# Kernel optimization log

Measured on AMD Instinct MI355X. Metric: run time of the kernel, lower is better.

## Reference

```python
import jax, jax.numpy as jnp
import numpy as np

NUM_EXECUTORS = 50
NUM_DAG_FEATURES = 3
EMB_DAG = 16
EMB_GLOB = 16
HIDDEN = [64, 64, 32]
B = 60000            # number of jobs (one per env in the batched rollout)
NODES_PER_JOB = 10
NODE_FEAT = 5


def _init_mlp(key, dims):
    ws, bs = [], []
    for i in range(len(dims) - 1):
        key, k = jax.random.split(key)
        scale = 1.0 / np.sqrt(dims[i])
        ws.append(jax.random.uniform(k, (dims[i], dims[i + 1]), jnp.float32, -scale, scale))
        bs.append(jnp.zeros((dims[i + 1],), jnp.float32))
    return ws, bs


def setup_inputs() -> dict:
    rng = np.random.default_rng(0)
    n_nodes = B * NODES_PER_JOB
    # dag_batch.ptr: job i owns nodes [i*NODES_PER_JOB, (i+1)*NODES_PER_JOB)
    ptr = np.arange(B + 1, dtype=np.int64) * NODES_PER_JOB
    job_indices = rng.permutation(B).astype(np.int64)
    # ragged action counts per job (exec_mask is a prefix mask of length num_exec_acts[i])
    num_exec_acts = rng.integers(1, NUM_EXECUTORS + 1, size=B).astype(np.int64)
    n_sel = num_exec_acts[job_indices]
    T = int(n_sel.sum())
    # per-ragged-row executor index: concat([arange(n) for n in n_sel]), vectorized
    starts = np.cumsum(n_sel) - n_sel
    exec_act_idx = (np.arange(T, dtype=np.int64) - np.repeat(starts, n_sel)).astype(np.int64)

    key = jax.random.key(0)
    k_x, k_hd, k_hg, k_mlp = jax.random.split(key, 4)
    x = jax.random.normal(k_x, (n_nodes, NODE_FEAT), jnp.float32)
    h_dag = jax.random.normal(k_hd, (B, EMB_DAG), jnp.float32)
    h_glob = jax.random.normal(k_hg, (B, EMB_GLOB), jnp.float32)

    in_dim = NUM_DAG_FEATURES + EMB_DAG + EMB_GLOB + 1  # 36
    ws, bs = _init_mlp(k_mlp, [in_dim] + HIDDEN + [1])

    return {
        "x": x,
        "h_dag": h_dag,
        "h_glob": h_glob,
        "ptr": jnp.asarray(ptr),
        "job_indices": jnp.asarray(job_indices),
        "num_exec_acts": jnp.asarray(num_exec_acts),
        "exec_act_idx": jnp.asarray(exec_act_idx),
        "W1": ws[0], "b1": bs[0],
        "W2": ws[1], "b2": bs[1],
        "W3": ws[2], "b3": bs[2],
        "W4": ws[3], "b4": bs[3],
    }


def reference(x, h_dag, h_glob, ptr, job_indices, num_exec_acts, exec_act_idx,
              W1, b1, W2, b2, W3, b3, W4, b4):
    T = exec_act_idx.shape[0]                       # total ragged action rows (static)
    J = job_indices.shape[0]
    # masked gather: dag features at each dag's start node, then select jobs
    x_dag = x[ptr[:-1], :NUM_DAG_FEATURES][job_indices]        # [J, 3]
    h_dag_sel = h_dag[job_indices]                              # [J, 16]
    x_h_dag = jnp.concatenate([x_dag, h_dag_sel], axis=1)       # [J, 19]
    # variable repeat_interleave -> gather by repeated row index
    n_sel = num_exec_acts[job_indices]
    rpt = jnp.repeat(jnp.arange(J), n_sel, total_repeat_length=T)
    x_h_rpt = x_h_dag[rpt]                                      # [T, 19]
    h_glob_rpt = h_glob[rpt]                                    # [T, 16]
    # exec action feature: k / num_executors for the k-th valid executor
    exec_actions = (exec_act_idx.astype(x.dtype) / NUM_EXECUTORS)[:, None]  # [T, 1]
    h = jnp.concatenate([x_h_rpt, h_glob_rpt, exec_actions], axis=1)        # [T, 36]
    h = jax.nn.relu(h @ W1 + b1)
    h = jax.nn.relu(h @ W2 + b2)
    h = jax.nn.relu(h @ W3 + b3)
    scores = (h @ W4 + b4).squeeze(-1)                          # [T]
    return scores
```

## Files before the change

### kernel.cpp

```cpp
#include <hip/hip_runtime.h>

#define TPB 256

using half8  = __attribute__((ext_vector_type(8))) _Float16;
using fp16x2 = __attribute__((ext_vector_type(2))) __fp16;
using hv2    = __attribute__((ext_vector_type(2))) _Float16;
using f32x4  = __attribute__((ext_vector_type(4))) float;

static __device__ __forceinline__ unsigned pkrtz(float a, float b) {
    fp16x2 h = __builtin_amdgcn_cvt_pkrtz(a, b);
    return __builtin_bit_cast(unsigned, h);
}
static __device__ __forceinline__ hv2 pk2(float a, float b) {
    fp16x2 h = __builtin_amdgcn_cvt_pkrtz(a, b);
    return __builtin_bit_cast(hv2, h);
}
template <int CTRL>
static __device__ __forceinline__ float dppmov(float x) {
    return __int_as_float(__builtin_amdgcn_mov_dpp(__float_as_int(x), CTRL, 0xF, 0xF, true));
}
#define DPP_SWAP 0xB1

__global__ __launch_bounds__(TPB) void k_prep(const float* __restrict__ x,
                                              const float* __restrict__ h_dag,
                                              const float* __restrict__ h_glob,
                                              const int* __restrict__ ptr,
                                              const int* __restrict__ job_indices,
                                              const int* __restrict__ num_exec_acts,
                                              int J, int nb,
                                              unsigned* __restrict__ s16,
                                              int* __restrict__ bsum, int* __restrict__ jsv,
                                              const float* __restrict__ W1,
                                              const float* __restrict__ b1,
                                              const float* __restrict__ W2,
                                              const float* __restrict__ b2,
                                              const float* __restrict__ W3,
                                              const float* __restrict__ b3,
                                              const float* __restrict__ W4,
                                              uint4* __restrict__ wfrag,
                                              float4* __restrict__ bfrag)
{
    if (blockIdx.x == (unsigned)(4 * nb)) {
        if (threadIdx.x < 64) {
            int lane = threadIdx.x;
            int n = lane & 15, q = lane >> 4;
#pragma unroll
            for (int nt = 0; nt < 4; nt++) {
#pragma unroll
                for (int s = 0; s < 2; s++) {
                    half8 w2f;
#pragma unroll
                    for (int jj = 0; jj < 8; jj++) {
                        int ks = s * 32 + q * 8 + jj;
                        w2f[jj] = (_Float16)W2[ks * 64 + nt * 16 + n];
                    }
                    wfrag[(8 + nt * 2 + s) * 64 + lane] = __builtin_bit_cast(uint4, w2f);
                }
            }
#pragma unroll
            for (int nt = 0; nt < 2; nt++) {
#pragma unroll
                for (int s = 0; s < 2; s++) {
                    half8 w3f;
#pragma unroll
                    for (int jj = 0; jj < 8; jj++) {
                        int ks = s * 32 + q * 8 + jj;
                        w3f[jj] = (_Float16)W3[ks * 32 + nt * 16 + n];
                    }
                    wfrag[(16 + nt * 2 + s) * 64 + lane] = __builtin_bit_cast(uint4, w3f);
                }
            }
            bfrag[1 * 64 + lane] = make_float4(b2[n], b2[16 + n], b2[32 + n], b2[48 + n]);
            bfrag[2 * 64 + lane] = make_float4(b3[n], b3[16 + n], W4[n], W4[16 + n]);
        }
        return;
    }

    const int qtr = blockIdx.x / nb;
    const int cb  = blockIdx.x - qtr * nb;
    int j = cb * TPB + threadIdx.x;
    int v = 0;
    if (j < J) {
        int ji   = job_indices[j];
        if (qtr == 0) v = num_exec_acts[ji];
        int node = ptr[ji];
        float f[35];
        f[0] = x[node * 5 + 0];
        f[1] = x[node * 5 + 1];
        f[2] = x[node * 5 + 2];
        float4 hd[4], hg[4];
#pragma unroll
        for (int c4 = 0; c4 < 4; c4++) hd[c4] = *(const float4*)(h_dag + (size_t)ji * 16 + 4 * c4);
#pragma unroll
        for (int c4 = 0; c4 < 4; c4++) hg[c4] = *(const float4*)(h_glob + (size_t)j * 16 + 4 * c4);
#pragma unroll
        for (int c4 = 0; c4 < 4; c4++) {
            f[3 + 4 * c4 + 0]  = hd[c4].x; f[3 + 4 * c4 + 1]  = hd[c4].y;
            f[3 + 4 * c4 + 2]  = hd[c4].z; f[3 + 4 * c4 + 3]  = hd[c4].w;
            f[19 + 4 * c4 + 0] = hg[c4].x; f[19 + 4 * c4 + 1] = hg[c4].y;
            f[19 + 4 * c4 + 2] = hg[c4].z; f[19 + 4 * c4 + 3] = hg[c4].w;
        }
        float acc[16];
#pragma unroll
        for (int d4 = 0; d4 < 4; d4++) {
            float4 b = *(const float4*)(b1 + qtr * 16 + 4 * d4);
            acc[4 * d4 + 0] = b.x; acc[4 * d4 + 1] = b.y;
            acc[4 * d4 + 2] = b.z; acc[4 * d4 + 3] = b.w;
        }
#pragma unroll
        for (int c = 0; c < 35; c++) {
            float fc = f[c];
#pragma unroll
            for (int d4 = 0; d4 < 4; d4++) {
                float4 w = *(const float4*)(W1 + c * 64 + qtr * 16 + 4 * d4);
                acc[4 * d4 + 0] += fc * w.x; acc[4 * d4 + 1] += fc * w.y;
                acc[4 * d4 + 2] += fc * w.z; acc[4 * d4 + 3] += fc * w.w;
            }
        }
        unsigned* dst = s16 + ((size_t)qtr * J + j) * 8;
        ((uint4*)dst)[0] = make_uint4(pkrtz(acc[0], acc[1]),  pkrtz(acc[2], acc[3]),
                                      pkrtz(acc[4], acc[5]),  pkrtz(acc[6], acc[7]));
        ((uint4*)dst)[1] = make_uint4(pkrtz(acc[8], acc[9]),  pkrtz(acc[10], acc[11]),
                                      pkrtz(acc[12], acc[13]), pkrtz(acc[14], acc[15]));
    }
    if (qtr != 0) return;

    __shared__ int sc[TPB];
    sc[threadIdx.x] = v;
    __syncthreads();
    for (int d = 1; d < TPB; d <<= 1) {
        int add = (threadIdx.x >= d) ? sc[threadIdx.x - d] : 0;
        __syncthreads();
        sc[threadIdx.x] += add;
        __syncthreads();
    }
    if (j < J) jsv[j] = ((sc[threadIdx.x] - v) << 6) | v;
    if (threadIdx.x == TPB - 1) bsum[cb] = sc[TPB - 1];
}

__global__ __launch_bounds__(TPB) void k_mlp_mfma(const unsigned* __restrict__ s16,
                                                  const float* __restrict__ W1,
                                                  const int* __restrict__ jsv,
                                                  const int* __restrict__ bsum,
                                                  const uint4* __restrict__ wfrag,
                                                  const float4* __restrict__ bfrag,
                                                  const float* __restrict__ b4,
                                                  float* __restrict__ out,
                                                  int T, int J, int nb, int numTiles, int chunk)
{
    __shared__ __align__(16) char smem[4 * 4096];
    __shared__ int boffs[TPB];
    __shared__ int swin[4][64];
    __shared__ int srow[4][64];
    const int tid  = threadIdx.x;
    const int lane = tid & 63;
    const int wv   = tid >> 6;
    const int n    = lane & 15;
    const int q    = lane >> 4;
    char* slab = smem + wv * 4096;

    {
        int v = (tid < nb) ? bsum[tid] : 0;
        boffs[tid] = v;
        __syncthreads();
        for (int d = 1; d < TPB; d <<= 1) {
            int add = (tid >= d) ? boffs[tid - d] : 0;
            __syncthreads();
            boffs[tid] += add;
            __syncthreads();
        }
        int ex = boffs[tid] - v;
        __syncthreads();
        boffs[tid] = ex;
        __syncthreads();
    }

    half8 bw2[4][2], bw3[2][2];
#pragma unroll
    for (int nt = 0; nt < 4; nt++)
#pragma unroll
        for (int s = 0; s < 2; s++)
            bw2[nt][s] = __builtin_bit_cast(half8, wfrag[(8 + nt * 2 + s) * 64 + lane]);
#pragma unroll
    for (int nt = 0; nt < 2; nt++)
#pragma unroll
        for (int s = 0; s < 2; s++)
            bw3[nt][s] = __builtin_bit_cast(half8, wfrag[(16 + nt * 2 + s) * 64 + lane]);

    float4 bf2 = bfrag[1 * 64 + lane];
    float4 bf3 = bfrag[2 * 64 + lane];
    float bb2[4] = {bf2.x, bf2.y, bf2.z, bf2.w};
    float bb3[2] = {bf3.x, bf3.y};
    const float w4a = bf3.z, w4b = bf3.w;
    const float b4v = b4[0];
    const int   swr = (n >> 1) & 7;
    const int   odd = n & 1;

    hv2 w36p[8];
    {
        const float* wp = W1 + 35 * 64 + q * 8;
#pragma unroll
        for (int k = 0; k < 4; k++) w36p[k]     = pk2(wp[2 * k],      wp[2 * k + 1]);
#pragma unroll
        for (int k = 0; k < 4; k++) w36p[4 + k] = pk2(wp[32 + 2 * k], wp[32 + 2 * k + 1]);
    }
    const hv2 z2 = {(_Float16)0.0f, (_Float16)0.0f};

    const uint4* sbLo = (const uint4*)s16 + ((size_t)(q >> 1) * J) * 2 + (q & 1);
    const uint4* sbHi = (const uint4*)s16 + ((size_t)(2 + (q >> 1)) * J) * 2 + (q & 1);

    const int t0 = blockIdx.x * chunk;
    const int t1 = (t0 + chunk < numTiles) ? (t0 + chunk) : numTiles;
    const int R  = (t1 - t0) * 32;
    const int r0 = t0 * 128 + wv * R;
    int rend = r0 + R;
    if (rend > T) rend = T;

    if (r0 < rend) {
        int j_lo;
        {
            int lo = 0, hi = nb - 1;
            while (lo < hi) {
                int mid = (lo + hi + 1) >> 1;
                if (boffs[mid] <= r0) lo = mid; else hi = mid - 1;
            }
            j_lo = lo << 8;
        }
        int sreg    = 0;
        int win_top = 0x80000000;

        half8 a2[2][2];

        auto build_a2 = [&](int mtbase) {
#pragma unroll
            for (int m = 0; m < 2; m++) {
                int u   = srow[wv][16 * (mtbase + m) + n];
                int job = u >> 8;
                float e = (float)(u & 255) * 0.02f;
                uint4 lo = sbLo[(size_t)job * 2];
                uint4 hi = sbHi[(size_t)job * 2];
                hv2 epk = pk2(e, e);
                hv2 r0_ = __builtin_elementwise_max(__builtin_bit_cast(hv2, lo.x) + epk * w36p[0], z2);
                hv2 r1_ = __builtin_elementwise_max(__builtin_bit_cast(hv2, lo.y) + epk * w36p[1], z2);
                hv2 r2_ = __builtin_elementwise_max(__builtin_bit_cast(hv2, lo.z) + epk * w36p[2], z2);
                hv2 r3_ = __builtin_elementwise_max(__builtin_bit_cast(hv2, lo.w) + epk * w36p[3], z2);
                a2[m][0] = __builtin_bit_cast(half8, make_uint4(__builtin_bit_cast(unsigned, r0_),
                                                                __builtin_bit_cast(unsigned, r1_),
                                                                __builtin_bit_cast(unsigned, r2_),
                                                                __builtin_bit_cast(unsigned, r3_)));
                hv2 r4_ = __builtin_elementwise_max(__builtin_bit_cast(hv2, hi.x) + epk * w36p[4], z2);
                hv2 r5_ = __builtin_elementwise_max(__builtin_bit_cast(hv2, hi.y) + epk * w36p[5], z2);
                hv2 r6_ = __builtin_elementwise_max(__builtin_bit_cast(hv2, hi.z) + epk * w36p[6], z2);
                hv2 r7_ = __builtin_elementwise_max(__builtin_bit_cast(hv2, hi.w) + epk * w36p[7], z2);
                a2[m][1] = __builtin_bit_cast(half8, make_uint4(__builtin_bit_cast(unsigned, r4_),
                                                                __builtin_bit_cast(unsigned, r5_),
                                                                __builtin_bit_cast(unsigned, r6_),
                                                                __builtin_bit_cast(unsigned, r7_)));
            }
        };

        auto stage_L2r = [&]() {
#pragma unroll
            for (int mt = 0; mt < 2; mt++) {
                f32x4 acc[4];
#pragma unroll
                for (int nt = 0; nt < 4; nt++) { f32x4 c; c[0]=c[1]=c[2]=c[3]=bb2[nt]; acc[nt]=c; }
#pragma unroll
                for (int s = 0; s < 2; s++) {
#pragma unroll
                    for (int nt = 0; nt < 4; nt++)
                        acc[nt] = __builtin_amdgcn_mfma_f32_16x16x32_f16(a2[mt][s], bw2[nt][s], acc[nt], 0, 0, 0);
                }
                unsigned* sl = (unsigned*)slab;
#pragma unroll
                for (int nt = 0; nt < 4; nt++) {
                    float v0 = fmaxf(acc[nt][0], 0.0f), v1 = fmaxf(acc[nt][1], 0.0f);
                    float v2 = fmaxf(acc[nt][2], 0.0f), v3 = fmaxf(acc[nt][3], 0.0f);
                    float t0_ = dppmov<DPP_SWAP>(v0), t1_ = dppmov<DPP_SWAP>(v1);
                    float t2_ = dppmov<DPP_SWAP>(v2), t3_ = dppmov<DPP_SWAP>(v3);
                    unsigned u0 = pkrtz(odd ? t2_ : v0, odd ? v2 : t0_);
                    unsigned u1 = pkrtz(odd ? t3_ : v1, odd ? v3 : t1_);
                    int rowA = 16 * mt + 4 * q + (odd ? 2 : 0);
                    int c    = 2 * nt + (n >> 3);
                    int a0   = (rowA * 8 + (c ^ ((rowA >> 1) & 7))) * 4 + ((n >> 1) & 3);
                    sl[a0] = u0; sl[a0 + 32] = u1;
                }
            }
        };

        auto stage_L34 = [&](int rbb) {
#pragma unroll
            for (int mt = 0; mt < 2; mt++) {
                const int M0 = 16 * mt;
                f32x4 acc[2];
#pragma unroll
                for (int nt = 0; nt < 2; nt++) { f32x4 c; c[0]=c[1]=c[2]=c[3]=bb3[nt]; acc[nt]=c; }
#pragma unroll
                for (int s = 0; s < 2; s++) {
                    half8 a = *(const half8*)(slab + ((M0 + n) * 8 + ((s * 4 + q) ^ swr)) * 16);
#pragma unroll
                    for (int nt = 0; nt < 2; nt++)
                        acc[nt] = __builtin_amdgcn_mfma_f32_16x16x32_f16(a, bw3[nt][s], acc[nt], 0, 0, 0);
                }
                f32x4 red;
#pragma unroll
                for (int r = 0; r < 4; r++)
                    red[r] = fmaxf(acc[0][r], 0.0f) * w4a + fmaxf(acc[1][r], 0.0f) * w4b;
#pragma unroll
                for (int r = 0; r < 4; r++) {
                    red[r] += dppmov<0x121>(red[r]);
                    red[r] += dppmov<0x122>(red[r]);
                    red[r] += dppmov<0x124>(red[r]);
                    red[r] += dppmov<0x128>(red[r]);
                }
                int t = rbb + M0 + q * 4 + n;
                float val = (n == 0) ? red[0] : (n == 1) ? red[1] : (n == 2) ? red[2] : red[3];
                if (n < 4 && t < T) out[t] = val + b4v;
            }
        };

        for (int rb = r0; rb < rend; rb += 64) {
            if (win_top <= rb + 63) {
                for (;;) {
                    int jj = j_lo + lane;
                    sreg = (jj < J) ? (boffs[jj >> 8] + (jsv[jj] >> 6)) : 0x7fffffff;
                    unsigned long long m = __ballot(sreg <= rb);
                    int adv = 63 - __builtin_clzll(m);
                    j_lo += adv;
                    if (adv == 0) break;
                }
                swin[wv][lane] = sreg;
                win_top = __shfl(sreg, 63);
            }

            {
                int rt = rb + lane;
                const int* sw = swin[wv];
                int lj = 0;
#pragma unroll
                for (int stp = 32; stp; stp >>= 1) {
                    int c2 = lj + stp;
                    if (c2 < 64 && sw[c2] <= rt) lj = c2;
                }
                int job = j_lo + lj;
                if (job > J - 1) job = J - 1;
                srow[wv][lane] = (job << 8) | (rt - sw[lj]);
            }

            build_a2(0);
            stage_L2r();
            stage_L34(rb);
            if (rb + 32 < rend) {
                build_a2(2);
                stage_L2r();
                stage_L34(rb + 32);
            }
        }
    }
}

extern "C" void kernel_launch(void* const* d_in, const int* in_sizes, int n_in,
                              void* d_out, int out_size, void* d_ws, size_t ws_size,
                              hipStream_t stream)
{
    const float* x             = (const float*)d_in[0];
    const float* h_dag         = (const float*)d_in[1];
    const float* h_glob        = (const float*)d_in[2];
    const int*   ptr           = (const int*)d_in[3];
    const int*   job_indices   = (const int*)d_in[4];
    const int*   num_exec_acts = (const int*)d_in[5];
    const float* W1 = (const float*)d_in[7];
    const float* b1 = (const float*)d_in[8];
    const float* W2 = (const float*)d_in[9];
    const float* b2 = (const float*)d_in[10];
    const float* W3 = (const float*)d_in[11];
    const float* b3 = (const float*)d_in[12];
    const float* W4 = (const float*)d_in[13];
    const float* b4 = (const float*)d_in[14];
    float* out = (float*)d_out;

    int J  = in_sizes[4];
    int T  = in_sizes[6];
    int nb = (J + TPB - 1) / TPB;

    char* wsp = (char*)d_ws;
    int* bsum = (int*)wsp;
    wsp += (((size_t)nb * 4) + 255) / 256 * 256;
    int* jsv = (int*)wsp;
    wsp += (((size_t)J * 4) + 255) / 256 * 256;
    uint4* wfrag = (uint4*)wsp;
    wsp += 20 * 64 * 16;
    float4* bfrag = (float4*)wsp;
    wsp += 3 * 64 * 16;
    unsigned* s16 = (unsigned*)wsp;

    k_prep<<<4 * nb + 1, TPB, 0, stream>>>(x, h_dag, h_glob, ptr, job_indices, num_exec_acts,
                                           J, nb, s16, bsum, jsv,
                                           W1, b1, W2, b2, W3, b3, W4, wfrag, bfrag);

    int numTiles = (T + 127) / 128;
    int grid = numTiles < 2048 ? numTiles : 2048;
    int chunk = (numTiles + grid - 1) / grid;
    grid = (numTiles + chunk - 1) / chunk;
    k_mlp_mfma<<<grid, TPB, 0, stream>>>(s16, W1, jsv, bsum, wfrag, bfrag, b4,
                                         out, T, J, nb, numTiles, chunk);
}
```

Measured before the change: 153.3 us.

## Compute layer 2 transposed so its output feeds layer 3 MFMA from registers

Layer 2 now runs with swapped MFMA operands (weights as A, activations as B), and W2 columns are pre-permuted so each lane's accumulator outputs already form the A-operand fragment for layer 3. This removes the LDS round trip (DPP swaps, packed stores to a swizzled slab, reloads) between layers 2 and 3, along with the 16 KB shared slab. Per-lane bias vectors for layer 2 are loaded directly from b2 in the matching permuted order. The cost is extra registers for the bias vectors and a reliance on the permutation being exactly right for correctness.

```diff
diff --git a/kernel.cpp b/kernel.cpp
--- a/kernel.cpp
+++ b/kernel.cpp
@@ -19,7 +19,6 @@
 static __device__ __forceinline__ float dppmov(float x) {
     return __int_as_float(__builtin_amdgcn_mov_dpp(__float_as_int(x), CTRL, 0xF, 0xF, true));
 }
-#define DPP_SWAP 0xB1
 
 __global__ __launch_bounds__(TPB) void k_prep(const float* __restrict__ x,
                                               const float* __restrict__ h_dag,
@@ -46,13 +45,14 @@
             int n = lane & 15, q = lane >> 4;
 #pragma unroll
             for (int nt = 0; nt < 4; nt++) {
+                const int sig = 8 * (n >> 2) + (n & 3) + 4 * (nt & 1) + 32 * (nt >> 1);
 #pragma unroll
                 for (int s = 0; s < 2; s++) {
                     half8 w2f;
 #pragma unroll
                     for (int jj = 0; jj < 8; jj++) {
                         int ks = s * 32 + q * 8 + jj;
-                        w2f[jj] = (_Float16)W2[ks * 64 + nt * 16 + n];
+                        w2f[jj] = (_Float16)W2[ks * 64 + sig];
                     }
                     wfrag[(8 + nt * 2 + s) * 64 + lane] = __builtin_bit_cast(uint4, w2f);
                 }
@@ -70,7 +70,6 @@
                     wfrag[(16 + nt * 2 + s) * 64 + lane] = __builtin_bit_cast(uint4, w3f);
                 }
             }
-            bfrag[1 * 64 + lane] = make_float4(b2[n], b2[16 + n], b2[32 + n], b2[48 + n]);
             bfrag[2 * 64 + lane] = make_float4(b3[n], b3[16 + n], W4[n], W4[16 + n]);
         }
         return;
@@ -140,6 +139,7 @@
 
 __global__ __launch_bounds__(TPB) void k_mlp_mfma(const unsigned* __restrict__ s16,
                                                   const float* __restrict__ W1,
+                                                  const float* __restrict__ b2,
                                                   const int* __restrict__ jsv,
                                                   const int* __restrict__ bsum,
                                                   const uint4* __restrict__ wfrag,
@@ -148,7 +148,6 @@
                                                   float* __restrict__ out,
                                                   int T, int J, int nb, int numTiles, int chunk)
 {
-    __shared__ __align__(16) char smem[4 * 4096];
     __shared__ int boffs[TPB];
     __shared__ int swin[4][64];
     __shared__ int srow[4][64];
@@ -157,7 +156,6 @@
     const int wv   = tid >> 6;
     const int n    = lane & 15;
     const int q    = lane >> 4;
-    char* slab = smem + wv * 4096;
 
     {
         int v = (tid < nb) ? bsum[tid] : 0;
@@ -187,14 +185,15 @@
         for (int s = 0; s < 2; s++)
             bw3[nt][s] = __builtin_bit_cast(half8, wfrag[(16 + nt * 2 + s) * 64 + lane]);
 
-    float4 bf2 = bfrag[1 * 64 + lane];
+    float4 bb2q[4];
+#pragma unroll
+    for (int nt = 0; nt < 4; nt++)
+        bb2q[nt] = *(const float4*)(b2 + 8 * q + 4 * (nt & 1) + 32 * (nt >> 1));
+
     float4 bf3 = bfrag[2 * 64 + lane];
-    float bb2[4] = {bf2.x, bf2.y, bf2.z, bf2.w};
     float bb3[2] = {bf3.x, bf3.y};
     const float w4a = bf3.z, w4b = bf3.w;
     const float b4v = b4[0];
-    const int   swr = (n >> 1) & 7;
-    const int   odd = n & 1;
 
     hv2 w36p[8];
     {
@@ -259,64 +258,52 @@
             }
         };
 
-        auto stage_L2r = [&]() {
-#pragma unroll
-            for (int mt = 0; mt < 2; mt++) {
-                f32x4 acc[4];
-#pragma unroll
-                for (int nt = 0; nt < 4; nt++) { f32x4 c; c[0]=c[1]=c[2]=c[3]=bb2[nt]; acc[nt]=c; }
-#pragma unroll
-                for (int s = 0; s < 2; s++) {
-#pragma unroll
-                    for (int nt = 0; nt < 4; nt++)
-                        acc[nt] = __builtin_amdgcn_mfma_f32_16x16x32_f16(a2[mt][s], bw2[nt][s], acc[nt], 0, 0, 0);
-                }
-                unsigned* sl = (unsigned*)slab;
-#pragma unroll
-                for (int nt = 0; nt < 4; nt++) {
-                    float v0 = fmaxf(acc[nt][0], 0.0f), v1 = fmaxf(acc[nt][1], 0.0f);
-                    float v2 = fmaxf(acc[nt][2], 0.0f), v3 = fmaxf(acc[nt][3], 0.0f);
-                    float t0_ = dppmov<DPP_SWAP>(v0), t1_ = dppmov<DPP_SWAP>(v1);
-                    float t2_ = dppmov<DPP_SWAP>(v2), t3_ = dppmov<DPP_SWAP>(v3);
-                    unsigned u0 = pkrtz(odd ? t2_ : v0, odd ? v2 : t0_);
-                    unsigned u1 = pkrtz(odd ? t3_ : v1, odd ? v3 : t1_);
-                    int rowA = 16 * mt + 4 * q + (odd ? 2 : 0);
-                    int c    = 2 * nt + (n >> 3);
-                    int a0   = (rowA * 8 + (c ^ ((rowA >> 1) & 7))) * 4 + ((n >> 1) & 3);
-                    sl[a0] = u0; sl[a0 + 32] = u1;
-                }
-            }
-        };
-
-        auto stage_L34 = [&](int rbb) {
-#pragma unroll
-            for (int mt = 0; mt < 2; mt++) {
-                const int M0 = 16 * mt;
-                f32x4 acc[2];
-#pragma unroll
-                for (int nt = 0; nt < 2; nt++) { f32x4 c; c[0]=c[1]=c[2]=c[3]=bb3[nt]; acc[nt]=c; }
-#pragma unroll
-                for (int s = 0; s < 2; s++) {
-                    half8 a = *(const half8*)(slab + ((M0 + n) * 8 + ((s * 4 + q) ^ swr)) * 16);
-#pragma unroll
-                    for (int nt = 0; nt < 2; nt++)
-                        acc[nt] = __builtin_amdgcn_mfma_f32_16x16x32_f16(a, bw3[nt][s], acc[nt], 0, 0, 0);
-                }
-                f32x4 red;
-#pragma unroll
-                for (int r = 0; r < 4; r++)
-                    red[r] = fmaxf(acc[0][r], 0.0f) * w4a + fmaxf(acc[1][r], 0.0f) * w4b;
-#pragma unroll
-                for (int r = 0; r < 4; r++) {
-                    red[r] += dppmov<0x121>(red[r]);
-                    red[r] += dppmov<0x122>(red[r]);
-                    red[r] += dppmov<0x124>(red[r]);
-                    red[r] += dppmov<0x128>(red[r]);
-                }
-                int t = rbb + M0 + q * 4 + n;
-                float val = (n == 0) ? red[0] : (n == 1) ? red[1] : (n == 2) ? red[2] : red[3];
-                if (n < 4 && t < T) out[t] = val + b4v;
-            }
+        auto process_mt = [&](int mt, int rbb) {
+            f32x4 acc2[4];
+#pragma unroll
+            for (int nt = 0; nt < 4; nt++) {
+                f32x4 c; c[0] = bb2q[nt].x; c[1] = bb2q[nt].y; c[2] = bb2q[nt].z; c[3] = bb2q[nt].w;
+                acc2[nt] = c;
+            }
+#pragma unroll
+            for (int s = 0; s < 2; s++)
+#pragma unroll
+                for (int nt = 0; nt < 4; nt++)
+                    acc2[nt] = __builtin_amdgcn_mfma_f32_16x16x32_f16(bw2[nt][s], a2[mt][s], acc2[nt], 0, 0, 0);
+
+            half8 a3[2];
+#pragma unroll
+            for (int s = 0; s < 2; s++) {
+                unsigned u0 = pkrtz(fmaxf(acc2[2 * s][0], 0.0f),     fmaxf(acc2[2 * s][1], 0.0f));
+                unsigned u1 = pkrtz(fmaxf(acc2[2 * s][2], 0.0f),     fmaxf(acc2[2 * s][3], 0.0f));
+                unsigned u2 = pkrtz(fmaxf(acc2[2 * s + 1][0], 0.0f), fmaxf(acc2[2 * s + 1][1], 0.0f));
+                unsigned u3 = pkrtz(fmaxf(acc2[2 * s + 1][2], 0.0f), fmaxf(acc2[2 * s + 1][3], 0.0f));
+                a3[s] = __builtin_bit_cast(half8, make_uint4(u0, u1, u2, u3));
+            }
+
+            f32x4 acc3[2];
+#pragma unroll
+            for (int nt2 = 0; nt2 < 2; nt2++) { f32x4 c; c[0]=c[1]=c[2]=c[3]=bb3[nt2]; acc3[nt2]=c; }
+#pragma unroll
+            for (int s = 0; s < 2; s++)
+#pragma unroll
+                for (int nt2 = 0; nt2 < 2; nt2++)
+                    acc3[nt2] = __builtin_amdgcn_mfma_f32_16x16x32_f16(a3[s], bw3[nt2][s], acc3[nt2], 0, 0, 0);
+
+            f32x4 red;
+#pragma unroll
+            for (int r = 0; r < 4; r++)
+                red[r] = fmaxf(acc3[0][r], 0.0f) * w4a + fmaxf(acc3[1][r], 0.0f) * w4b;
+#pragma unroll
+            for (int r = 0; r < 4; r++) {
+                red[r] += dppmov<0x121>(red[r]);
+                red[r] += dppmov<0x122>(red[r]);
+                red[r] += dppmov<0x124>(red[r]);
+                red[r] += dppmov<0x128>(red[r]);
+            }
+            int t = rbb + 16 * mt + q * 4 + n;
+            float val = (n == 0) ? red[0] : (n == 1) ? red[1] : (n == 2) ? red[2] : red[3];
+            if (n < 4 && t < T) out[t] = val + b4v;
         };
 
         for (int rb = r0; rb < rend; rb += 64) {
@@ -348,12 +335,12 @@
             }
 
             build_a2(0);
-            stage_L2r();
-            stage_L34(rb);
+            process_mt(0, rb);
+            process_mt(1, rb);
             if (rb + 32 < rend) {
                 build_a2(2);
-                stage_L2r();
-                stage_L34(rb + 32);
+                process_mt(0, rb + 32);
+                process_mt(1, rb + 32);
             }
         }
     }
@@ -402,6 +389,6 @@
     int grid = numTiles < 2048 ? numTiles : 2048;
     int chunk = (numTiles + grid - 1) / grid;
     grid = (numTiles + chunk - 1) / chunk;
-    k_mlp_mfma<<<grid, TPB, 0, stream>>>(s16, W1, jsv, bsum, wfrag, bfrag, b4,
+    k_mlp_mfma<<<grid, TPB, 0, stream>>>(s16, W1, b2, jsv, bsum, wfrag, bfrag, b4,
                                          out, T, J, nb, numTiles, chunk);
 }
```

After: 154.5 us. About the same (+0.7%).
